# Kernel tuning notes

Hardware: AMD Instinct MI355X
Metric: run time of the kernel (lower is better)

## Reference

```python
import jax, jax.numpy as jnp
import numpy as np

G, C, L, D, H, NCLS = 64, 32, 128, 64, 128, 10


def setup_inputs() -> dict:
    key = jax.random.key(0)
    ks = jax.random.split(key, 5)
    scale = 0.05
    return {
        "cycle_reps": jax.random.normal(ks[0], (G, C, L, D), dtype=jnp.float32),
        "W_ih": jax.random.normal(ks[1], (4 * H, D), dtype=jnp.float32) * scale,
        "W_hh": jax.random.normal(ks[2], (4 * H, H), dtype=jnp.float32) * scale,
        "b_ih": jnp.zeros((4 * H,), dtype=jnp.float32),
        "b_hh": jnp.zeros((4 * H,), dtype=jnp.float32),
        "W_cls": jax.random.normal(ks[3], (NCLS, H), dtype=jnp.float32) * scale,
        "b_cls": jnp.zeros((NCLS,), dtype=jnp.float32),
    }


def _lstm_seq_sum(x, W_ih, W_hh, b):
    """Run a single-layer LSTM over x [B, L, D]; return sum of hidden states over L -> [B, H]."""
    B = x.shape[0]
    Hh = W_hh.shape[1]
    # precompute input-side gate pre-activations for all timesteps: [L, B, 4H]
    xg = jnp.einsum('bld,gd->lbg', x, W_ih) + b

    def step(carry, xg_t):
        h, c = carry
        gates = xg_t + h @ W_hh.T  # [B, 4H]
        i, f, g, o = jnp.split(gates, 4, axis=-1)  # torch i/f/g/o gate order
        i = jax.nn.sigmoid(i)
        f = jax.nn.sigmoid(f)
        g = jnp.tanh(g)
        o = jax.nn.sigmoid(o)
        c = f * c + i * g
        h = o * jnp.tanh(c)
        return (h, c), h

    init = (jnp.zeros((B, Hh), x.dtype), jnp.zeros((B, Hh), x.dtype))
    _, hs = jax.lax.scan(step, init, xg)  # hs: [L, B, H]
    return hs.sum(axis=0)


def reference(cycle_reps, W_ih, W_hh, b_ih, b_hh, W_cls, b_cls):
    Gn, Cn, Ln, Dn = cycle_reps.shape
    x = cycle_reps.reshape(Gn * Cn, Ln, Dn)
    rep = _lstm_seq_sum(x, W_ih, W_hh, b_ih + b_hh)  # [G*C, H]: sum of LSTM outputs over seq
    rep = rep.reshape(Gn, Cn, -1)
    # torch.var_mean over the cycle axis; only the mean is used as the graph rep
    graph_mean = rep.mean(axis=1)  # [G, H]
    logits = graph_mean @ W_cls.T + b_cls  # classifier_gnn
    return jax.nn.log_softmax(logits, axis=1)
```

## Files before the change

kernel.cpp:

```cpp
#include <hip/hip_runtime.h>
#include <hip/hip_bf16.h>

#define NSEQ 2048
#define LSEQ 128
#define DIN  64
#define HID  128
#define NCLS 10

typedef __attribute__((ext_vector_type(8))) short bfrag8;
typedef __attribute__((ext_vector_type(4))) float facc4;

__device__ __forceinline__ short f2bf(float f) {
    union { __hip_bfloat16 b; short s; } u;
    u.b = __float2bfloat16(f);
    return u.s;
}

__device__ __forceinline__ bfrag8 load_bf16_frag(const float* __restrict__ p) {
    bfrag8 r;
#pragma unroll
    for (int j = 0; j < 8; ++j) r[j] = f2bf(p[j]);
    return r;
}

__device__ __forceinline__ float fast_sigmoid(float x) {
    float e = __builtin_amdgcn_exp2f(-1.4426950408889634f * x);
    return __builtin_amdgcn_rcpf(1.0f + e);
}
__device__ __forceinline__ float fast_tanh(float x) {
    float e = __builtin_amdgcn_exp2f(2.8853900817779268f * x);
    return 1.0f - 2.0f * __builtin_amdgcn_rcpf(1.0f + e);
}

__device__ __forceinline__ float lane_redistribute(float r_low, float r_high) {
    float d = r_low, s = r_high;
    asm("v_permlane32_swap_b32 %0, %1" : "+v"(d), "+v"(s));
    return d;
}

__device__ __forceinline__ void block_barrier() {
    asm volatile("s_waitcnt lgkmcnt(0)" ::: "memory");
    __builtin_amdgcn_s_barrier();
    asm volatile("" ::: "memory");
}

__global__ __launch_bounds__(1024) void lstm_fused(
    const float* __restrict__ x,
    const float* __restrict__ Wih,
    const float* __restrict__ Whh,
    const float* __restrict__ bih,
    const float* __restrict__ bhh,
    float* __restrict__ rep)
{
    __shared__ __align__(16) __hip_bfloat16 hbuf[2][8][136];
    __shared__ __align__(16) float xgbuf[3][512][8];
    __shared__ __align__(16) __hip_bfloat16 xstage[2][8][72];

    const int tid  = threadIdx.x;
    const int w    = tid >> 6;
    const int lane = tid & 63;
    const int ln   = lane & 15;
    const int qd   = lane >> 4;
    const int s0   = blockIdx.x * 8;

    if (w < 8) {
        const int khid = w * 16 + ln;
        const int sq0  = (qd & 1) * 4 + (qd >> 1) * 2;
        const int sq1  = sq0 + 1;

        bfrag8 whr[4][4];
#pragma unroll
        for (int g = 0; g < 4; ++g) {
            const int col = g * HID + khid;
#pragma unroll
            for (int k0 = 0; k0 < 4; ++k0)
                whr[g][k0] = load_bf16_frag(Whh + col * HID + k0 * 32 + qd * 8);
        }

        {
            unsigned int* ph = (unsigned int*)&hbuf[0][0][0];
            for (int i = tid; i < 2 * 8 * 136 / 2; i += 512) ph[i] = 0u;
        }

        float cst[2]  = {0.f, 0.f};
        float hsum[2] = {0.f, 0.f};

        block_barrier();

        const int xoff = khid * 8 + (qd & 1) * 4;
        facc4 acc[4];
#pragma unroll
        for (int g = 0; g < 4; ++g)
            acc[g] = *(const facc4*)(&xgbuf[0][0][0] + g * 1024 + xoff);

        int cur = 0, bufN = 1;
#pragma unroll 1
        for (int t = 0; t < LSEQ; ++t) {
            bfrag8 hf0 = *(const bfrag8*)(&hbuf[cur][ln & 7][qd * 8]);
            bfrag8 hf1 = *(const bfrag8*)(&hbuf[cur][ln & 7][32 + qd * 8]);
            bfrag8 hf2 = *(const bfrag8*)(&hbuf[cur][ln & 7][64 + qd * 8]);
            bfrag8 hf3 = *(const bfrag8*)(&hbuf[cur][ln & 7][96 + qd * 8]);
            __builtin_amdgcn_s_setprio(1);
#pragma unroll
            for (int g = 0; g < 4; ++g) {
                acc[g] = __builtin_amdgcn_mfma_f32_16x16x32_bf16(hf0, whr[g][0], acc[g], 0, 0, 0);
                acc[g] = __builtin_amdgcn_mfma_f32_16x16x32_bf16(hf1, whr[g][1], acc[g], 0, 0, 0);
                acc[g] = __builtin_amdgcn_mfma_f32_16x16x32_bf16(hf2, whr[g][2], acc[g], 0, 0, 0);
                acc[g] = __builtin_amdgcn_mfma_f32_16x16x32_bf16(hf3, whr[g][3], acc[g], 0, 0, 0);
            }
            __builtin_amdgcn_s_setprio(0);

            float u0[4], u1[4];
#pragma unroll
            for (int g = 0; g < 4; ++g) {
                u0[g] = lane_redistribute(acc[g][0], acc[g][2]);
                u1[g] = lane_redistribute(acc[g][1], acc[g][3]);
            }

            {
                const float* xgN = &xgbuf[bufN][0][0] + xoff;
#pragma unroll
                for (int g = 0; g < 4; ++g)
                    acc[g] = *(const facc4*)(xgN + g * 1024);
            }

            short hb[2];
#pragma unroll
            for (int j = 0; j < 2; ++j) {
                float iv = fast_sigmoid(j ? u1[0] : u0[0]);
                float fv = fast_sigmoid(j ? u1[1] : u0[1]);
                float gv = fast_tanh   (j ? u1[2] : u0[2]);
                float ov = fast_sigmoid(j ? u1[3] : u0[3]);
                float c  = fv * cst[j] + iv * gv;
                cst[j]   = c;
                float hv = ov * fast_tanh(c);
                hsum[j] += hv;
                hb[j]    = f2bf(hv);
            }
            ((short*)&hbuf[cur ^ 1][sq0][0])[khid] = hb[0];
            ((short*)&hbuf[cur ^ 1][sq1][0])[khid] = hb[1];

            block_barrier();
            cur ^= 1;
            bufN = (bufN == 2) ? 0 : bufN + 1;
        }

        rep[(size_t)(s0 + sq0) * HID + khid] = hsum[0];
        rep[(size_t)(s0 + sq1) * HID + khid] = hsum[1];
    } else {
        const int p = w - 8;
        const int colbase = p * 16 + ln;

        bfrag8 wir[4][2];
        facc4  biasf[4];
#pragma unroll
        for (int g = 0; g < 4; ++g) {
            const int col = g * HID + colbase;
            const float b = bih[col] + bhh[col];
            biasf[g] = (facc4){b, b, b, b};
#pragma unroll
            for (int k0 = 0; k0 < 2; ++k0)
                wir[g][k0] = load_bf16_frag(Wih + col * DIN + k0 * 32 + qd * 8);
        }

        const float* xr = x + (size_t)(s0 + (ln & 7)) * (LSEQ * DIN) + qd * 8;
#pragma unroll
        for (int tt = 0; tt < 2; ++tt) {
            float4 a00 = *(const float4*)(xr + tt * DIN);
            float4 a01 = *(const float4*)(xr + tt * DIN + 4);
            float4 a10 = *(const float4*)(xr + tt * DIN + 32);
            float4 a11 = *(const float4*)(xr + tt * DIN + 36);
            bfrag8 xf0, xf1;
#pragma unroll
            for (int j = 0; j < 4; ++j) {
                xf0[j] = f2bf(((float*)&a00)[j]); xf0[4 + j] = f2bf(((float*)&a01)[j]);
                xf1[j] = f2bf(((float*)&a10)[j]); xf1[4 + j] = f2bf(((float*)&a11)[j]);
            }
#pragma unroll
            for (int g = 0; g < 4; ++g) {
                facc4 a = __builtin_amdgcn_mfma_f32_16x16x32_bf16(xf0, wir[g][0], biasf[g], 0, 0, 0);
                a = __builtin_amdgcn_mfma_f32_16x16x32_bf16(xf1, wir[g][1], a, 0, 0, 0);
                if (qd < 2)
                    *(facc4*)(&xgbuf[tt][0][0] + (g * 128 + colbase) * 8 + qd * 4) = a;
            }
        }

        const float* xsrow = x + (size_t)(s0 + p) * (LSEQ * DIN) + lane;
        xstage[0][p][lane] = __float2bfloat16(xsrow[2 * DIN]);
        float xnext = xsrow[3 * DIN];

        block_barrier();

        int bufW = 2;
#pragma unroll 1
        for (int t = 0; t < LSEQ; ++t) {
            if (t < LSEQ - 2) {
                bfrag8 xf0 = *(const bfrag8*)(&xstage[(t + 2) & 1][ln & 7][qd * 8]);
                bfrag8 xf1 = *(const bfrag8*)(&xstage[(t + 2) & 1][ln & 7][32 + qd * 8]);
                if (t < LSEQ - 3) {
                    xstage[(t + 3) & 1][p][lane] = __float2bfloat16(xnext);
                    if (t < LSEQ - 4) xnext = xsrow[(t + 4) * DIN];
                }
#pragma unroll
                for (int g = 0; g < 4; ++g) {
                    facc4 a = __builtin_amdgcn_mfma_f32_16x16x32_bf16(xf0, wir[g][0], biasf[g], 0, 0, 0);
                    a = __builtin_amdgcn_mfma_f32_16x16x32_bf16(xf1, wir[g][1], a, 0, 0, 0);
                    if (qd < 2)
                        *(facc4*)(&xgbuf[bufW][0][0] + (g * 128 + colbase) * 8 + qd * 4) = a;
                }
            }
            block_barrier();
            bufW = (bufW == 2) ? 0 : bufW + 1;
        }
    }
}

__global__ __launch_bounds__(128) void cls_kernel(
    const float* __restrict__ rep,
    const float* __restrict__ Wcls,
    const float* __restrict__ bcls,
    float* __restrict__ out)
{
    __shared__ float m_s[HID];
    __shared__ float logits_s[NCLS];
    const int g = blockIdx.x;
    const int h = threadIdx.x;

    float s = 0.f;
#pragma unroll 4
    for (int c = 0; c < 32; ++c)
        s += rep[((size_t)g * 32 + c) * HID + h];
    m_s[h] = s * (1.0f / 32.0f);
    __syncthreads();

    if (h < NCLS) {
        float acc = bcls[h];
        for (int k = 0; k < HID; ++k)
            acc += m_s[k] * Wcls[h * HID + k];
        logits_s[h] = acc;
    }
    __syncthreads();

    if (h < NCLS) {
        float mx = logits_s[0];
#pragma unroll
        for (int j = 1; j < NCLS; ++j) mx = fmaxf(mx, logits_s[j]);
        float se = 0.f;
#pragma unroll
        for (int j = 0; j < NCLS; ++j)
            se += __builtin_amdgcn_exp2f((logits_s[j] - mx) * 1.4426950408889634f);
        float lse = mx + 0.6931471805599453f * __builtin_amdgcn_logf(se);
        out[g * NCLS + h] = logits_s[h] - lse;
    }
}

extern "C" void kernel_launch(void* const* d_in, const int* in_sizes, int n_in,
                              void* d_out, int out_size, void* d_ws, size_t ws_size,
                              hipStream_t stream) {
    const float* x    = (const float*)d_in[0];
    const float* Wih  = (const float*)d_in[1];
    const float* Whh  = (const float*)d_in[2];
    const float* bih  = (const float*)d_in[3];
    const float* bhh  = (const float*)d_in[4];
    const float* Wcls = (const float*)d_in[5];
    const float* bcls = (const float*)d_in[6];

    float* rep = (float*)d_ws;

    lstm_fused<<<NSEQ / 8, 1024, 0, stream>>>(x, Wih, Whh, bih, bhh, rep);
    cls_kernel<<<64, 128, 0, stream>>>(rep, Wcls, bcls, (float*)d_out);
}
```

Before: 203.7 us.

## Merge producer/consumer warps: compute input projection inline in recurrent warps

Drops the 8 producer warps that precomputed input-gate pre-activations into a triple-buffered LDS area. Each of the 8 recurrent warps now computes the x·W_ih MFMAs itself every step, fed by 16-step bf16 chunks of x that are prefetched from global and staged into double-buffered LDS. The W_hh product is split into two independent accumulator chains to shorten the dependency chain. Block size halves to 512 and LDS use shrinks, which could allow more resident blocks, but the per-step critical path in each warp gains eight extra MFMAs.

```diff
diff --git a/kernel.cpp b/kernel.cpp
--- a/kernel.cpp
+++ b/kernel.cpp
@@ -6,6 +6,8 @@
 #define DIN  64
 #define HID  128
 #define NCLS 10
+#define XPAD 72
+#define CHK  16
 
 typedef __attribute__((ext_vector_type(8))) short bfrag8;
 typedef __attribute__((ext_vector_type(4))) float facc4;
@@ -44,7 +46,7 @@
     asm volatile("" ::: "memory");
 }
 
-__global__ __launch_bounds__(1024) void lstm_fused(
+__global__ __launch_bounds__(512) void lstm_fused(
     const float* __restrict__ x,
     const float* __restrict__ Wih,
     const float* __restrict__ Whh,
@@ -53,8 +55,7 @@
     float* __restrict__ rep)
 {
     __shared__ __align__(16) __hip_bfloat16 hbuf[2][8][136];
-    __shared__ __align__(16) float xgbuf[3][512][8];
-    __shared__ __align__(16) __hip_bfloat16 xstage[2][8][72];
+    __shared__ __align__(16) __hip_bfloat16 xs[2][CHK][8][XPAD];
 
     const int tid  = threadIdx.x;
     const int w    = tid >> 6;
@@ -62,157 +63,136 @@
     const int ln   = lane & 15;
     const int qd   = lane >> 4;
     const int s0   = blockIdx.x * 8;
-
-    if (w < 8) {
-        const int khid = w * 16 + ln;
-        const int sq0  = (qd & 1) * 4 + (qd >> 1) * 2;
-        const int sq1  = sq0 + 1;
-
-        bfrag8 whr[4][4];
+    const int khid = w * 16 + ln;
+    const int sq0  = (qd & 1) * 4 + (qd >> 1) * 2;
+    const int sq1  = sq0 + 1;
+
+    bfrag8 whh[4][4];
+    bfrag8 wih[4][2];
+    facc4  biasf[4];
+#pragma unroll
+    for (int g = 0; g < 4; ++g) {
+        const int col = g * HID + khid;
+        const float b = bih[col] + bhh[col];
+        biasf[g] = (facc4){b, b, b, b};
+#pragma unroll
+        for (int k0 = 0; k0 < 4; ++k0)
+            whh[g][k0] = load_bf16_frag(Whh + col * HID + k0 * 32 + qd * 8);
+#pragma unroll
+        for (int k0 = 0; k0 < 2; ++k0)
+            wih[g][k0] = load_bf16_frag(Wih + col * DIN + k0 * 32 + qd * 8);
+    }
+
+    {
+        unsigned int* p = (unsigned int*)&hbuf[0][0][0];
+        for (int i = tid; i < 2 * 8 * 136 / 2; i += 512) p[i] = 0u;
+    }
+
+    const float* xsrc = x + (size_t)(s0 + w) * (LSEQ * DIN) + lane * 16;
+    const int stt = lane >> 2;
+    const int sdd = (lane & 3) * 16;
+
+    {
+        float4 a0 = ((const float4*)xsrc)[0];
+        float4 a1 = ((const float4*)xsrc)[1];
+        float4 a2 = ((const float4*)xsrc)[2];
+        float4 a3 = ((const float4*)xsrc)[3];
+        bfrag8 o0, o1;
+#pragma unroll
+        for (int j = 0; j < 4; ++j) { o0[j] = f2bf(((float*)&a0)[j]); o0[4+j] = f2bf(((float*)&a1)[j]); }
+#pragma unroll
+        for (int j = 0; j < 4; ++j) { o1[j] = f2bf(((float*)&a2)[j]); o1[4+j] = f2bf(((float*)&a3)[j]); }
+        *(bfrag8*)&xs[0][stt][w][sdd]     = o0;
+        *(bfrag8*)&xs[0][stt][w][sdd + 8] = o1;
+    }
+
+    float cst[2]  = {0.f, 0.f};
+    float hsum[2] = {0.f, 0.f};
+
+    block_barrier();
+
+    const facc4 zero4 = {0.f, 0.f, 0.f, 0.f};
+    float4 l0, l1, l2, l3;
+    int cur = 0;
+
+#pragma unroll 1
+    for (int t = 0; t < LSEQ; ++t) {
+        const int buf   = (t >> 4) & 1;
+        const int ct    = t & (CHK - 1);
+        const int chunk = t >> 4;
+        const bool more = chunk < (LSEQ / CHK - 1);
+
+        bfrag8 xf0 = *(const bfrag8*)(&xs[buf][ct][ln & 7][qd * 8]);
+        bfrag8 xf1 = *(const bfrag8*)(&xs[buf][ct][ln & 7][32 + qd * 8]);
+        bfrag8 hf0 = *(const bfrag8*)(&hbuf[cur][ln & 7][qd * 8]);
+        bfrag8 hf1 = *(const bfrag8*)(&hbuf[cur][ln & 7][32 + qd * 8]);
+        bfrag8 hf2 = *(const bfrag8*)(&hbuf[cur][ln & 7][64 + qd * 8]);
+        bfrag8 hf3 = *(const bfrag8*)(&hbuf[cur][ln & 7][96 + qd * 8]);
+
+        facc4 ax[4];
 #pragma unroll
         for (int g = 0; g < 4; ++g) {
-            const int col = g * HID + khid;
-#pragma unroll
-            for (int k0 = 0; k0 < 4; ++k0)
-                whr[g][k0] = load_bf16_frag(Whh + col * HID + k0 * 32 + qd * 8);
-        }
-
-        {
-            unsigned int* ph = (unsigned int*)&hbuf[0][0][0];
-            for (int i = tid; i < 2 * 8 * 136 / 2; i += 512) ph[i] = 0u;
-        }
-
-        float cst[2]  = {0.f, 0.f};
-        float hsum[2] = {0.f, 0.f};
+            ax[g] = __builtin_amdgcn_mfma_f32_16x16x32_bf16(xf0, wih[g][0], biasf[g], 0, 0, 0);
+            ax[g] = __builtin_amdgcn_mfma_f32_16x16x32_bf16(xf1, wih[g][1], ax[g], 0, 0, 0);
+        }
+
+        facc4 gt[4];
+#pragma unroll
+        for (int g = 0; g < 4; ++g) {
+            facc4 pa = __builtin_amdgcn_mfma_f32_16x16x32_bf16(hf0, whh[g][0], ax[g], 0, 0, 0);
+            pa = __builtin_amdgcn_mfma_f32_16x16x32_bf16(hf1, whh[g][1], pa, 0, 0, 0);
+            facc4 pb = __builtin_amdgcn_mfma_f32_16x16x32_bf16(hf2, whh[g][2], zero4, 0, 0, 0);
+            pb = __builtin_amdgcn_mfma_f32_16x16x32_bf16(hf3, whh[g][3], pb, 0, 0, 0);
+            gt[g] = pa + pb;
+        }
+
+        if (ct == 0 && more) {
+            const float* p = xsrc + (chunk + 1) * (CHK * DIN);
+            l0 = ((const float4*)p)[0];
+            l1 = ((const float4*)p)[1];
+            l2 = ((const float4*)p)[2];
+            l3 = ((const float4*)p)[3];
+        }
+
+        float u0[4], u1[4];
+#pragma unroll
+        for (int g = 0; g < 4; ++g) {
+            u0[g] = lane_redistribute(gt[g][0], gt[g][2]);
+            u1[g] = lane_redistribute(gt[g][1], gt[g][3]);
+        }
+
+        if (ct == 12 && more) {
+            bfrag8 o0, o1;
+#pragma unroll
+            for (int j = 0; j < 4; ++j) { o0[j] = f2bf(((float*)&l0)[j]); o0[4+j] = f2bf(((float*)&l1)[j]); }
+#pragma unroll
+            for (int j = 0; j < 4; ++j) { o1[j] = f2bf(((float*)&l2)[j]); o1[4+j] = f2bf(((float*)&l3)[j]); }
+            *(bfrag8*)&xs[buf ^ 1][stt][w][sdd]     = o0;
+            *(bfrag8*)&xs[buf ^ 1][stt][w][sdd + 8] = o1;
+        }
+
+        short hb[2];
+#pragma unroll
+        for (int j = 0; j < 2; ++j) {
+            float iv = fast_sigmoid(j ? u1[0] : u0[0]);
+            float fv = fast_sigmoid(j ? u1[1] : u0[1]);
+            float gv = fast_tanh   (j ? u1[2] : u0[2]);
+            float ov = fast_sigmoid(j ? u1[3] : u0[3]);
+            float c  = fv * cst[j] + iv * gv;
+            cst[j]   = c;
+            float hv = ov * fast_tanh(c);
+            hsum[j] += hv;
+            hb[j]    = f2bf(hv);
+        }
+        ((short*)&hbuf[cur ^ 1][sq0][0])[khid] = hb[0];
+        ((short*)&hbuf[cur ^ 1][sq1][0])[khid] = hb[1];
 
         block_barrier();
-
-        const int xoff = khid * 8 + (qd & 1) * 4;
-        facc4 acc[4];
-#pragma unroll
-        for (int g = 0; g < 4; ++g)
-            acc[g] = *(const facc4*)(&xgbuf[0][0][0] + g * 1024 + xoff);
-
-        int cur = 0, bufN = 1;
-#pragma unroll 1
-        for (int t = 0; t < LSEQ; ++t) {
-            bfrag8 hf0 = *(const bfrag8*)(&hbuf[cur][ln & 7][qd * 8]);
-            bfrag8 hf1 = *(const bfrag8*)(&hbuf[cur][ln & 7][32 + qd * 8]);
-            bfrag8 hf2 = *(const bfrag8*)(&hbuf[cur][ln & 7][64 + qd * 8]);
-            bfrag8 hf3 = *(const bfrag8*)(&hbuf[cur][ln & 7][96 + qd * 8]);
-            __builtin_amdgcn_s_setprio(1);
-#pragma unroll
-            for (int g = 0; g < 4; ++g) {
-                acc[g] = __builtin_amdgcn_mfma_f32_16x16x32_bf16(hf0, whr[g][0], acc[g], 0, 0, 0);
-                acc[g] = __builtin_amdgcn_mfma_f32_16x16x32_bf16(hf1, whr[g][1], acc[g], 0, 0, 0);
-                acc[g] = __builtin_amdgcn_mfma_f32_16x16x32_bf16(hf2, whr[g][2], acc[g], 0, 0, 0);
-                acc[g] = __builtin_amdgcn_mfma_f32_16x16x32_bf16(hf3, whr[g][3], acc[g], 0, 0, 0);
-            }
-            __builtin_amdgcn_s_setprio(0);
-
-            float u0[4], u1[4];
-#pragma unroll
-            for (int g = 0; g < 4; ++g) {
-                u0[g] = lane_redistribute(acc[g][0], acc[g][2]);
-                u1[g] = lane_redistribute(acc[g][1], acc[g][3]);
-            }
-
-            {
-                const float* xgN = &xgbuf[bufN][0][0] + xoff;
-#pragma unroll
-                for (int g = 0; g < 4; ++g)
-                    acc[g] = *(const facc4*)(xgN + g * 1024);
-            }
-
-            short hb[2];
-#pragma unroll
-            for (int j = 0; j < 2; ++j) {
-                float iv = fast_sigmoid(j ? u1[0] : u0[0]);
-                float fv = fast_sigmoid(j ? u1[1] : u0[1]);
-                float gv = fast_tanh   (j ? u1[2] : u0[2]);
-                float ov = fast_sigmoid(j ? u1[3] : u0[3]);
-                float c  = fv * cst[j] + iv * gv;
-                cst[j]   = c;
-                float hv = ov * fast_tanh(c);
-                hsum[j] += hv;
-                hb[j]    = f2bf(hv);
-            }
-            ((short*)&hbuf[cur ^ 1][sq0][0])[khid] = hb[0];
-            ((short*)&hbuf[cur ^ 1][sq1][0])[khid] = hb[1];
-
-            block_barrier();
-            cur ^= 1;
-            bufN = (bufN == 2) ? 0 : bufN + 1;
-        }
-
-        rep[(size_t)(s0 + sq0) * HID + khid] = hsum[0];
-        rep[(size_t)(s0 + sq1) * HID + khid] = hsum[1];
-    } else {
-        const int p = w - 8;
-        const int colbase = p * 16 + ln;
-
-        bfrag8 wir[4][2];
-        facc4  biasf[4];
-#pragma unroll
-        for (int g = 0; g < 4; ++g) {
-            const int col = g * HID + colbase;
-            const float b = bih[col] + bhh[col];
-            biasf[g] = (facc4){b, b, b, b};
-#pragma unroll
-            for (int k0 = 0; k0 < 2; ++k0)
-                wir[g][k0] = load_bf16_frag(Wih + col * DIN + k0 * 32 + qd * 8);
-        }
-
-        const float* xr = x + (size_t)(s0 + (ln & 7)) * (LSEQ * DIN) + qd * 8;
-#pragma unroll
-        for (int tt = 0; tt < 2; ++tt) {
-            float4 a00 = *(const float4*)(xr + tt * DIN);
-            float4 a01 = *(const float4*)(xr + tt * DIN + 4);
-            float4 a10 = *(const float4*)(xr + tt * DIN + 32);
-            float4 a11 = *(const float4*)(xr + tt * DIN + 36);
-            bfrag8 xf0, xf1;
-#pragma unroll
-            for (int j = 0; j < 4; ++j) {
-                xf0[j] = f2bf(((float*)&a00)[j]); xf0[4 + j] = f2bf(((float*)&a01)[j]);
-                xf1[j] = f2bf(((float*)&a10)[j]); xf1[4 + j] = f2bf(((float*)&a11)[j]);
-            }
-#pragma unroll
-            for (int g = 0; g < 4; ++g) {
-                facc4 a = __builtin_amdgcn_mfma_f32_16x16x32_bf16(xf0, wir[g][0], biasf[g], 0, 0, 0);
-                a = __builtin_amdgcn_mfma_f32_16x16x32_bf16(xf1, wir[g][1], a, 0, 0, 0);
-                if (qd < 2)
-                    *(facc4*)(&xgbuf[tt][0][0] + (g * 128 + colbase) * 8 + qd * 4) = a;
-            }
-        }
-
-        const float* xsrow = x + (size_t)(s0 + p) * (LSEQ * DIN) + lane;
-        xstage[0][p][lane] = __float2bfloat16(xsrow[2 * DIN]);
-        float xnext = xsrow[3 * DIN];
-
-        block_barrier();
-
-        int bufW = 2;
-#pragma unroll 1
-        for (int t = 0; t < LSEQ; ++t) {
-            if (t < LSEQ - 2) {
-                bfrag8 xf0 = *(const bfrag8*)(&xstage[(t + 2) & 1][ln & 7][qd * 8]);
-                bfrag8 xf1 = *(const bfrag8*)(&xstage[(t + 2) & 1][ln & 7][32 + qd * 8]);
-                if (t < LSEQ - 3) {
-                    xstage[(t + 3) & 1][p][lane] = __float2bfloat16(xnext);
-                    if (t < LSEQ - 4) xnext = xsrow[(t + 4) * DIN];
-                }
-#pragma unroll
-                for (int g = 0; g < 4; ++g) {
-                    facc4 a = __builtin_amdgcn_mfma_f32_16x16x32_bf16(xf0, wir[g][0], biasf[g], 0, 0, 0);
-                    a = __builtin_amdgcn_mfma_f32_16x16x32_bf16(xf1, wir[g][1], a, 0, 0, 0);
-                    if (qd < 2)
-                        *(facc4*)(&xgbuf[bufW][0][0] + (g * 128 + colbase) * 8 + qd * 4) = a;
-                }
-            }
-            block_barrier();
-            bufW = (bufW == 2) ? 0 : bufW + 1;
-        }
-    }
+        cur ^= 1;
+    }
+
+    rep[(size_t)(s0 + sq0) * HID + khid] = hsum[0];
+    rep[(size_t)(s0 + sq1) * HID + khid] = hsum[1];
 }
 
 __global__ __launch_bounds__(128) void cls_kernel(
@@ -267,6 +247,6 @@
 
     float* rep = (float*)d_ws;
 
-    lstm_fused<<<NSEQ / 8, 1024, 0, stream>>>(x, Wih, Whh, bih, bhh, rep);
+    lstm_fused<<<NSEQ / 8, 512, 0, stream>>>(x, Wih, Whh, bih, bhh, rep);
     cls_kernel<<<64, 128, 0, stream>>>(rep, Wcls, bcls, (float*)d_out);
 }
```

Result: slower. 217.7 us (+6.9%).
